# Performance work log

Hardware: AMD Instinct MI355X
Metric: run time of the kernel (lower is better)

## Reference

```python
import jax, jax.numpy as jnp
import numpy as np

NX = 1024
NF = 4096
B = 8
S = 4096

def setup_inputs() -> dict:
    key = jax.random.key(0)
    k1, k2, k3, k4 = jax.random.split(key, 4)
    x = jax.random.normal(k1, (B, S, NX), dtype=jnp.float32)
    # symmetric int8 weights in [-127, 127]
    qw = jax.random.randint(k2, (NX, NF), -127, 128, dtype=jnp.int32).astype(jnp.int8)
    weight_scale = jax.random.uniform(k3, (), dtype=jnp.float32) * 0.01 + 1e-4
    bias = jax.random.normal(k4, (NF,), dtype=jnp.float32)
    return {"x": x, "quantized_weight": qw, "weight_scale": weight_scale, "bias": bias}

def reference(x, quantized_weight, weight_scale, bias):
    # dequantize: (int8 -> fp32) * scale, zero_point = 0
    w = quantized_weight.astype(jnp.float32) * weight_scale  # [nx, nf]
    size_out = x.shape[:-1] + (w.shape[-1],)
    out = x.reshape(-1, x.shape[-1]) @ w + bias               # addmm
    return out.reshape(size_out)
```

## Files before the change

kernel.cpp:

```cpp
#include <hip/hip_runtime.h>
#include <hip/hip_bf16.h>
#include <stdint.h>
#include <stddef.h>

typedef __bf16 bf16_t;
typedef __attribute__((ext_vector_type(8))) __bf16 bf16x8;
typedef __attribute__((ext_vector_type(4))) __bf16 bf16x4;
typedef __attribute__((ext_vector_type(4))) float f32x4;
typedef __attribute__((ext_vector_type(4))) int i32x4;
typedef __attribute__((ext_vector_type(16))) char c8x16;

#define M_DIM 32768
#define N_DIM 4096
#define K_DIM 1024
#define NT 16

static __device__ __forceinline__ void gload16(const void* g, void* s) {
  __builtin_amdgcn_global_load_lds(
      (const __attribute__((address_space(1))) void*)g,
      (__attribute__((address_space(3))) void*)s,
      16, 0, 0);
}

__global__ void quant_x_kernel(const float* __restrict__ x,
                               int8_t* __restrict__ xq,
                               float* __restrict__ xs) {
  const int row = blockIdx.x * 4 + (threadIdx.x >> 6);
  const int lane = threadIdx.x & 63;
  const float* src = x + (long)row * K_DIM + lane * 16;
  float4 v[4];
#pragma unroll
  for (int i = 0; i < 4; ++i) v[i] = ((const float4*)src)[i];
  float am = 0.f;
#pragma unroll
  for (int i = 0; i < 4; ++i) {
    am = fmaxf(am, fmaxf(fmaxf(fabsf(v[i].x), fabsf(v[i].y)),
                         fmaxf(fabsf(v[i].z), fabsf(v[i].w))));
  }
#pragma unroll
  for (int off = 32; off; off >>= 1) am = fmaxf(am, __shfl_xor(am, off));
  const float sq = am > 0.f ? 127.f / am : 0.f;
  c8x16 q;
#pragma unroll
  for (int i = 0; i < 4; ++i) {
    const float* f = (const float*)&v[i];
#pragma unroll
    for (int j = 0; j < 4; ++j) {
      int qi = (int)rintf(f[j] * sq);
      qi = qi > 127 ? 127 : (qi < -127 ? -127 : qi);
      q[i * 4 + j] = (char)qi;
    }
  }
  *(c8x16*)(xq + (long)row * K_DIM + lane * 16) = q;
  if (lane == 0) xs[row] = am * (1.f / 127.f);
}

__global__ void cvt_w_i8_kernel(const int* __restrict__ qw,
                                int8_t* __restrict__ wq) {
  __shared__ char t[64][80];
  const int bk = blockIdx.x & 15;
  const int bn = blockIdx.x >> 4;
  const int k0 = bk * 64, n0 = bn * 64;
  const int tid = threadIdx.x;
  {
    const int kl = tid >> 2;
    const int nc = (tid & 3) * 16;
    const int* src = qw + (long)(k0 + kl) * N_DIM + n0 + nc;
#pragma unroll
    for (int c = 0; c < 4; ++c) {
      i32x4 v = *(const i32x4*)(src + c * 4);
#pragma unroll
      for (int j = 0; j < 4; ++j) t[nc + c * 4 + j][kl] = (char)v[j];
    }
  }
  __syncthreads();
  {
    const int nl = tid >> 2;
    const int kc = (tid & 3) * 16;
    *(i32x4*)(wq + (long)(n0 + nl) * K_DIM + k0 + kc) =
        *(const i32x4*)&t[nl][kc];
  }
}

__global__ __launch_bounds__(256, 4) void gemm_i8_kernel(
    const int8_t* __restrict__ Aq, const int8_t* __restrict__ Bq,
    const float* __restrict__ xs, const float* __restrict__ scale_p,
    const float* __restrict__ bias, float* __restrict__ C) {
  __shared__ __align__(16) char lds[32768];

  const int xcd = blockIdx.x & 7;
  const int slot = blockIdx.x >> 3;
  const int tn = (xcd << 2) | (slot & 3);
  const int tm = slot >> 2;

  const int tid = threadIdx.x;
  const int wave = tid >> 6;
  const int lane = tid & 63;
  const int lr = lane & 15;
  const int lg = lane >> 4;
  const int wm = wave >> 1;
  const int wn = wave & 1;

  const long aRow0 = (long)tm * 128;
  const long bRow0 = (long)tn * 128;

  const int sr = tid >> 2;
  const int r0 = ((sr >> 5) << 6) + (sr & 31);
  const int sc = (((tid & 3) ^ ((tid >> 3) & 3)) << 4);
  const int8_t* aS = Aq + (aRow0 + r0) * K_DIM + sc;
  const int8_t* bS = Bq + (bRow0 + r0) * K_DIM + sc;
  char* sBase = lds + wave * 1024;

#define STG_A(b, h, t) \
  gload16(aS + (long)((h) * 32) * K_DIM + (t) * 64, sBase + (b) * 16384 + (h) * 4096)
#define STG_B(b, h, t) \
  gload16(bS + (long)((h) * 32) * K_DIM + (t) * 64, sBase + (b) * 16384 + 8192 + (h) * 4096)

  const int ck = ((lg ^ ((lr >> 1) & 3)) << 4);

#define LDA(m)                                                             \
  (*(const i32x4*)(lds + bb + ((m) >> 1) * 4096 +                          \
                   (wm * 32 + ((m) & 1) * 16 + lr) * 64 + ck))
#define LDB(n)                                                             \
  (*(const i32x4*)(lds + bb + 8192 + ((n) >> 1) * 4096 +                   \
                   (wn * 32 + ((n) & 1) * 16 + lr) * 64 + ck))

#define SYNC(Nimm)                                           \
  do {                                                       \
    asm volatile("s_waitcnt vmcnt(" #Nimm ")" ::: "memory"); \
    __builtin_amdgcn_s_barrier();                            \
    __builtin_amdgcn_sched_barrier(0);                       \
  } while (0)

  i32x4 acc[4][4] = {};
  i32x4 afr[4], bfr[4];

#define MFMA_Q(mb, nb)                                                        \
  do {                                                                        \
    __builtin_amdgcn_s_setprio(1);                                            \
    _Pragma("unroll") for (int mm = 0; mm < 2; ++mm)                          \
    _Pragma("unroll") for (int nn = 0; nn < 2; ++nn)                          \
      acc[(mb) + mm][(nb) + nn] = __builtin_amdgcn_mfma_i32_16x16x64_i8(      \
          afr[(mb) + mm], bfr[(nb) + nn], acc[(mb) + mm][(nb) + nn], 0, 0, 0);\
    __builtin_amdgcn_s_setprio(0);                                            \
  } while (0)

#define RD_B01() \
  _Pragma("unroll") for (int n = 0; n < 2; ++n) bfr[n] = LDB(n);
#define RD_B23() \
  _Pragma("unroll") for (int n = 2; n < 4; ++n) bfr[n] = LDB(n);
#define RD_A01() \
  _Pragma("unroll") for (int m = 0; m < 2; ++m) afr[m] = LDA(m);
#define RD_A23() \
  _Pragma("unroll") for (int m = 2; m < 4; ++m) afr[m] = LDA(m);

  STG_A(0, 0, 0);
  STG_B(0, 0, 0);
  STG_B(0, 1, 0);
  STG_A(0, 1, 0);

#pragma unroll 1
  for (int t = 0; t < NT - 1; ++t) {
    const int b = t & 1;
    const int nb = b ^ 1;
    const int bb = b * 16384;
    SYNC(2);
    RD_B01();
    RD_A01();
    STG_A(nb, 0, t + 1);
    MFMA_Q(0, 0);
    SYNC(2);
    RD_B23();
    STG_B(nb, 0, t + 1);
    MFMA_Q(0, 2);
    SYNC(2);
    RD_A23();
    STG_B(nb, 1, t + 1);
    MFMA_Q(2, 0);
    STG_A(nb, 1, t + 1);
    MFMA_Q(2, 2);
  }
  {
    const int bb = 16384;
    SYNC(2);
    RD_B01();
    RD_A01();
    MFMA_Q(0, 0);
    SYNC(1);
    RD_B23();
    MFMA_Q(0, 2);
    SYNC(0);
    RD_A23();
    MFMA_Q(2, 0);
    MFMA_Q(2, 2);
  }

#undef STG_A
#undef STG_B
#undef LDA
#undef LDB
#undef SYNC
#undef MFMA_Q
#undef RD_B01
#undef RD_B23
#undef RD_A01
#undef RD_A23

  const float ws = *scale_p;
  const int col_base = (tn << 7) + wn * 64;
  const int row_base = (tm << 7) + wm * 64 + lg * 4;
  float4 svw[4];
#pragma unroll
  for (int m = 0; m < 4; ++m) {
    float4 sv = *(const float4*)(xs + row_base + m * 16);
    svw[m].x = sv.x * ws; svw[m].y = sv.y * ws;
    svw[m].z = sv.z * ws; svw[m].w = sv.w * ws;
  }
#pragma unroll
  for (int n = 0; n < 4; ++n) {
    const int col = col_base + n * 16 + lr;
    const float bv = bias[col];
#pragma unroll
    for (int m = 0; m < 4; ++m) {
      float* cp = C + (long)(row_base + m * 16) * N_DIM + col;
      const float* sw = (const float*)&svw[m];
#pragma unroll
      for (int j = 0; j < 4; ++j)
        __builtin_nontemporal_store((float)acc[m][n][j] * sw[j] + bv,
                                    cp + (long)j * N_DIM);
    }
  }
}

__global__ void cvt_w_kernel(const int* __restrict__ qw, bf16_t* __restrict__ wt) {
  __shared__ bf16_t t[64][72];
  const int bk = blockIdx.x & 15;
  const int bn = blockIdx.x >> 4;
  const int k0 = bk * 64, n0 = bn * 64;
  const int tid = threadIdx.x;
  {
    const int kl = tid >> 2;
    const int nc = (tid & 3) * 16;
    const int* src = qw + (long)(k0 + kl) * N_DIM + n0 + nc;
#pragma unroll
    for (int c = 0; c < 4; ++c) {
      i32x4 v = *(const i32x4*)(src + c * 4);
#pragma unroll
      for (int j = 0; j < 4; ++j)
        t[nc + c * 4 + j][kl] = (bf16_t)(float)v[j];
    }
  }
  __syncthreads();
  {
    const int nl = tid >> 2;
    const int kc = (tid & 3) * 16;
    bf16_t* dst = wt + (long)(n0 + nl) * K_DIM + k0 + kc;
#pragma unroll
    for (int j = 0; j < 16; ++j) dst[j] = t[nl][kc + j];
  }
}

__global__ __launch_bounds__(256, 2) void gemm_fb_kernel(
    const float* __restrict__ Af, const bf16_t* __restrict__ Bt,
    const float* __restrict__ scale_p, const float* __restrict__ bias,
    float* __restrict__ C) {
  __shared__ bf16_t lA[128][64];
  __shared__ bf16_t lB[128][64];
  const int nwg = gridDim.x;
  int wg = blockIdx.x;
  wg = (wg & 7) * (nwg >> 3) + (wg >> 3);
  const int tm = wg & 255;
  const int tn = wg >> 8;
  const int tid = threadIdx.x;
  const int wave = tid >> 6;
  const int lane = tid & 63;
  const int lr = lane & 15;
  const int lg = lane >> 4;
  const int wm = wave >> 1;
  const int wn = wave & 1;
  const long aRow0 = (long)tm * 128;
  const long bRow0 = (long)tn * 128;
  const bf16_t* bSrc = Bt + (bRow0 + (tid >> 3)) * K_DIM + (tid & 7) * 8;
  char* ldsB = (char*)&lB[0][0] + wave * 1024;
  f32x4 acc[4][4] = {};
  for (int k0 = 0; k0 < K_DIM; k0 += 64) {
    __syncthreads();
#pragma unroll
    for (int j = 0; j < 8; ++j) {
      const int e = j * 1024 + tid * 4;
      const int row = e >> 6;
      const int col = e & 63;
      float4 v = *(const float4*)(Af + (aRow0 + row) * K_DIM + k0 + col);
      bf16x4 o;
      o[0] = (__bf16)v.x; o[1] = (__bf16)v.y; o[2] = (__bf16)v.z; o[3] = (__bf16)v.w;
      *(bf16x4*)((char*)&lA[0][0] + (size_t)e * 2) = o;
    }
#pragma unroll
    for (int i = 0; i < 4; ++i)
      gload16(bSrc + (long)i * 32 * K_DIM + k0, ldsB + i * 4096);
    __syncthreads();
#pragma unroll
    for (int kk = 0; kk < 2; ++kk) {
      bf16x8 af[4], bg[4];
#pragma unroll
      for (int m = 0; m < 4; ++m)
        af[m] = *(const bf16x8*)&lA[wm * 64 + m * 16 + lr][kk * 32 + lg * 8];
#pragma unroll
      for (int n = 0; n < 4; ++n)
        bg[n] = *(const bf16x8*)&lB[wn * 64 + n * 16 + lr][kk * 32 + lg * 8];
#pragma unroll
      for (int m = 0; m < 4; ++m)
#pragma unroll
        for (int n = 0; n < 4; ++n)
          acc[m][n] = __builtin_amdgcn_mfma_f32_16x16x32_bf16(af[m], bg[n], acc[m][n], 0, 0, 0);
    }
  }
  const float s = *scale_p;
  const int col0 = (tn << 7) + wn * 64;
  const int row0 = (tm << 7) + wm * 64 + lg * 4;
#pragma unroll
  for (int n = 0; n < 4; ++n) {
    const int col = col0 + n * 16 + lr;
    const float bv = bias[col];
#pragma unroll
    for (int m = 0; m < 4; ++m) {
      float* cp = C + (long)(row0 + m * 16) * N_DIM + col;
#pragma unroll
      for (int j = 0; j < 4; ++j)
        cp[(long)j * N_DIM] = acc[m][n][j] * s + bv;
    }
  }
}

extern "C" void kernel_launch(void* const* d_in, const int* in_sizes, int n_in,
                              void* d_out, int out_size, void* d_ws, size_t ws_size,
                              hipStream_t stream) {
  const float* x = (const float*)d_in[0];
  const int* qw = (const int*)d_in[1];
  const float* scale = (const float*)d_in[2];
  const float* bias = (const float*)d_in[3];
  float* out = (float*)d_out;

  const size_t wq_bytes = (size_t)N_DIM * K_DIM;
  const size_t xs_off = wq_bytes;
  const size_t xq_off = wq_bytes + (256u << 10);
  const size_t need = xq_off + (size_t)M_DIM * K_DIM;

  if (ws_size >= need) {
    int8_t* wq = (int8_t*)d_ws;
    float* xs = (float*)((char*)d_ws + xs_off);
    int8_t* xq = (int8_t*)((char*)d_ws + xq_off);
    cvt_w_i8_kernel<<<dim3((K_DIM / 64) * (N_DIM / 64)), dim3(256), 0, stream>>>(qw, wq);
    quant_x_kernel<<<dim3(M_DIM / 4), dim3(256), 0, stream>>>(x, xq, xs);
    gemm_i8_kernel<<<dim3((M_DIM / 128) * (N_DIM / 128)), dim3(256), 0, stream>>>(
        xq, wq, xs, scale, bias, out);
  } else {
    bf16_t* wt = (bf16_t*)d_ws;
    cvt_w_kernel<<<dim3((K_DIM / 64) * (N_DIM / 64)), dim3(256), 0, stream>>>(qw, wt);
    gemm_fb_kernel<<<dim3((M_DIM / 128) * (N_DIM / 128)), dim3(256), 0, stream>>>(
        x, wt, scale, bias, out);
  }
}
```

Before: 230.8 us.

## Double K-tile depth to 128 per stage with wider LDS swizzle

Raises the per-stage K slice of the int8 GEMM from 64 to 128, halving the number of main-loop iterations and barriers. LDS doubles to 64KB, staging issues two global-to-LDS loads per half-tile, and the XOR swizzle widens to 8 chunks across 128-byte rows. Each quarter-step now does two MFMAs per accumulator. The cost is lower occupancy (launch bounds 4 to 2 blocks per CU) and more fragment registers.

Result: faster. 209.0 us (-9.4%).

```diff
diff --git a/kernel.cpp b/kernel.cpp
--- a/kernel.cpp
+++ b/kernel.cpp
@@ -13,7 +13,7 @@
 #define M_DIM 32768
 #define N_DIM 4096
 #define K_DIM 1024
-#define NT 16
+#define NT 8
 
 static __device__ __forceinline__ void gload16(const void* g, void* s) {
   __builtin_amdgcn_global_load_lds(
@@ -82,11 +82,11 @@
   }
 }
 
-__global__ __launch_bounds__(256, 4) void gemm_i8_kernel(
+__global__ __launch_bounds__(256, 2) void gemm_i8_kernel(
     const int8_t* __restrict__ Aq, const int8_t* __restrict__ Bq,
     const float* __restrict__ xs, const float* __restrict__ scale_p,
     const float* __restrict__ bias, float* __restrict__ C) {
-  __shared__ __align__(16) char lds[32768];
+  __shared__ __align__(16) char lds[65536];
 
   const int xcd = blockIdx.x & 7;
   const int slot = blockIdx.x >> 3;
@@ -104,26 +104,38 @@
   const long aRow0 = (long)tm * 128;
   const long bRow0 = (long)tn * 128;
 
-  const int sr = tid >> 2;
-  const int r0 = ((sr >> 5) << 6) + (sr & 31);
-  const int sc = (((tid & 3) ^ ((tid >> 3) & 3)) << 4);
-  const int8_t* aS = Aq + (aRow0 + r0) * K_DIM + sc;
-  const int8_t* bS = Bq + (bRow0 + r0) * K_DIM + sc;
+  const int s = tid >> 3;
+  const int scol = ((tid & 7) ^ (s & 7)) * 16;
+  const int8_t* aS = Aq + (aRow0 + s) * K_DIM + scol;
+  const int8_t* bS = Bq + (bRow0 + s) * K_DIM + scol;
   char* sBase = lds + wave * 1024;
 
-#define STG_A(b, h, t) \
-  gload16(aS + (long)((h) * 32) * K_DIM + (t) * 64, sBase + (b) * 16384 + (h) * 4096)
-#define STG_B(b, h, t) \
-  gload16(bS + (long)((h) * 32) * K_DIM + (t) * 64, sBase + (b) * 16384 + 8192 + (h) * 4096)
-
-  const int ck = ((lg ^ ((lr >> 1) & 3)) << 4);
-
-#define LDA(m)                                                             \
-  (*(const i32x4*)(lds + bb + ((m) >> 1) * 4096 +                          \
-                   (wm * 32 + ((m) & 1) * 16 + lr) * 64 + ck))
-#define LDB(n)                                                             \
-  (*(const i32x4*)(lds + bb + 8192 + ((n) >> 1) * 4096 +                   \
-                   (wn * 32 + ((n) & 1) * 16 + lr) * 64 + ck))
+#define STG_A(b, h, t)                                                      \
+  do {                                                                      \
+    gload16(aS + (long)((h) * 32) * K_DIM + (t) * 128,                      \
+            sBase + (b) * 32768 + (h) * 8192);                              \
+    gload16(aS + (long)((h) * 32 + 64) * K_DIM + (t) * 128,                 \
+            sBase + (b) * 32768 + (h) * 8192 + 4096);                       \
+  } while (0)
+#define STG_B(b, h, t)                                                      \
+  do {                                                                      \
+    gload16(bS + (long)((h) * 32) * K_DIM + (t) * 128,                      \
+            sBase + (b) * 32768 + 16384 + (h) * 8192);                      \
+    gload16(bS + (long)((h) * 32 + 64) * K_DIM + (t) * 128,                 \
+            sBase + (b) * 32768 + 16384 + (h) * 8192 + 4096);               \
+  } while (0)
+
+  const int ck0 = ((0 + lg) ^ (lr & 7)) << 4;
+  const int ck1 = ((4 + lg) ^ (lr & 7)) << 4;
+
+#define LDA(m, kk)                                                           \
+  (*(const i32x4*)(lds + bb + ((m) >> 1) * 8192 +                            \
+                   (wm * 32 + ((m) & 1) * 16 + lr) * 128 +                   \
+                   ((kk) ? ck1 : ck0)))
+#define LDB(n, kk)                                                           \
+  (*(const i32x4*)(lds + bb + 16384 + ((n) >> 1) * 8192 +                    \
+                   (wn * 32 + ((n) & 1) * 16 + lr) * 128 +                   \
+                   ((kk) ? ck1 : ck0)))
 
 #define SYNC(Nimm)                                           \
   do {                                                       \
@@ -133,26 +145,41 @@
   } while (0)
 
   i32x4 acc[4][4] = {};
-  i32x4 afr[4], bfr[4];
-
-#define MFMA_Q(mb, nb)                                                        \
+  i32x4 bfr[4][2], afr[2][2];
+
+#define MFMA_Q(mbase, nbase)                                                  \
   do {                                                                        \
     __builtin_amdgcn_s_setprio(1);                                            \
     _Pragma("unroll") for (int mm = 0; mm < 2; ++mm)                          \
     _Pragma("unroll") for (int nn = 0; nn < 2; ++nn)                          \
-      acc[(mb) + mm][(nb) + nn] = __builtin_amdgcn_mfma_i32_16x16x64_i8(      \
-          afr[(mb) + mm], bfr[(nb) + nn], acc[(mb) + mm][(nb) + nn], 0, 0, 0);\
+    _Pragma("unroll") for (int kk = 0; kk < 2; ++kk)                          \
+      acc[(mbase) + mm][(nbase) + nn] =                                       \
+          __builtin_amdgcn_mfma_i32_16x16x64_i8(                              \
+              afr[mm][kk], bfr[(nbase) + nn][kk],                             \
+              acc[(mbase) + mm][(nbase) + nn], 0, 0, 0);                      \
     __builtin_amdgcn_s_setprio(0);                                            \
   } while (0)
 
-#define RD_B01() \
-  _Pragma("unroll") for (int n = 0; n < 2; ++n) bfr[n] = LDB(n);
-#define RD_B23() \
-  _Pragma("unroll") for (int n = 2; n < 4; ++n) bfr[n] = LDB(n);
-#define RD_A01() \
-  _Pragma("unroll") for (int m = 0; m < 2; ++m) afr[m] = LDA(m);
-#define RD_A23() \
-  _Pragma("unroll") for (int m = 2; m < 4; ++m) afr[m] = LDA(m);
+#define RD_B01()                                                              \
+  _Pragma("unroll") for (int n = 0; n < 2; ++n) {                             \
+    bfr[n][0] = LDB(n, 0);                                                    \
+    bfr[n][1] = LDB(n, 1);                                                    \
+  }
+#define RD_B23()                                                              \
+  _Pragma("unroll") for (int n = 2; n < 4; ++n) {                             \
+    bfr[n][0] = LDB(n, 0);                                                    \
+    bfr[n][1] = LDB(n, 1);                                                    \
+  }
+#define RD_A01()                                                              \
+  _Pragma("unroll") for (int mm = 0; mm < 2; ++mm) {                          \
+    afr[mm][0] = LDA(mm, 0);                                                  \
+    afr[mm][1] = LDA(mm, 1);                                                  \
+  }
+#define RD_A23()                                                              \
+  _Pragma("unroll") for (int mm = 0; mm < 2; ++mm) {                          \
+    afr[mm][0] = LDA(mm + 2, 0);                                              \
+    afr[mm][1] = LDA(mm + 2, 1);                                              \
+  }
 
   STG_A(0, 0, 0);
   STG_B(0, 0, 0);
@@ -163,17 +190,17 @@
   for (int t = 0; t < NT - 1; ++t) {
     const int b = t & 1;
     const int nb = b ^ 1;
-    const int bb = b * 16384;
-    SYNC(2);
+    const int bb = b * 32768;
+    SYNC(4);
     RD_B01();
     RD_A01();
     STG_A(nb, 0, t + 1);
     MFMA_Q(0, 0);
-    SYNC(2);
+    SYNC(4);
     RD_B23();
     STG_B(nb, 0, t + 1);
     MFMA_Q(0, 2);
-    SYNC(2);
+    SYNC(4);
     RD_A23();
     STG_B(nb, 1, t + 1);
     MFMA_Q(2, 0);
@@ -181,12 +208,12 @@
     MFMA_Q(2, 2);
   }
   {
-    const int bb = 16384;
-    SYNC(2);
+    const int bb = 32768;
+    SYNC(4);
     RD_B01();
     RD_A01();
     MFMA_Q(0, 0);
-    SYNC(1);
+    SYNC(2);
     RD_B23();
     MFMA_Q(0, 2);
     SYNC(0);
```
